# Kernel optimization log

Hardware: AMD Instinct MI355X
Metric: run time of the kernel (lower is better)

Reference implementation:

```python
import jax, jax.numpy as jnp
import numpy as np

LAGRANGE_ORDER = 5  # fixed, as in the torch module


def _lagrange_weights(alpha):
    """Vectorised Lagrange weights of length L+1. alpha: [B,N] -> [B,N,L+1]."""
    L = LAGRANGE_ORDER
    j = jnp.arange(L + 1, dtype=alpha.dtype)
    u = alpha[..., None] - j                          # [B,N,L+1]
    denom = j[:, None] - j[None, :]                   # [L+1,L+1]
    mask = ~jnp.eye(L + 1, dtype=bool)
    num = jnp.where(mask, u[..., None, :], jnp.ones_like(u)[..., None, :])
    den = jnp.where(mask, denom, jnp.ones_like(denom))
    return (num / den).prod(axis=-1)                  # [B,N,L+1]


def setup_inputs() -> dict:
    key = jax.random.key(0)
    k1, k2, k3 = jax.random.split(key, 3)
    B, N = 16, 16384
    # fractional period in samples, in [40, 100) -> max floor(f0)=99, K=99+5+3=107<=108
    f0 = 40.0 + 60.0 * jax.random.uniform(k1, (B, N), dtype=jnp.float32)
    x = jax.random.normal(k2, (B, N), dtype=jnp.float32)
    l_b = jax.random.uniform(k3, (B, N, 2), dtype=jnp.float32)  # (g, p) in [0,1]
    return {"f0": f0, "x": x, "l_b": l_b, "K": 108}


def reference(f0, x, l_b, K):
    B, N = x.shape
    L = LAGRANGE_ORDER
    # design_loop: (g, p) -> loop taps [b0, a1]; gain capped <1 for stability
    g = 0.99 * l_b[..., 0]
    p = l_b[..., 1]
    b0 = g * (1.0 - p)                                # [B,N]
    a1 = g * p
    # tune_f0: subtract low-frequency phase delay of (b0 + a1 z^-1)
    f0c = f0 - a1 / (b0 + a1 + 1e-7)
    # Lagrange centre & weights
    z = jnp.floor(f0c).astype(jnp.int32)
    z_center = z - L // 2                             # [B,N]
    alpha = f0c - z_center.astype(f0.dtype)
    w = _lagrange_weights(alpha)                      # [B,N,L+1]
    # compute_resonator_matrix: loop filter convolved with fractional delay -> block [B,N,L+2]
    block = (b0[..., None] * jnp.pad(w, ((0, 0), (0, 0), (0, 1)))
             + a1[..., None] * jnp.pad(w, ((0, 0), (0, 0), (1, 0))))
    # scatter (-block) into A; LPC lag k+1 lives in column k
    cols = z_center[..., None] - 1 + jnp.arange(L + 2)  # [B,N,L+2]
    cols = jnp.clip(cols, 0, K - 1)
    A = jnp.zeros((B, N, K), x.dtype).at[
        jnp.arange(B)[:, None, None], jnp.arange(N)[None, :, None], cols
    ].add(-block)
    # sample_wise_lpc: y[n] = x[n] - sum_k A[n,k] * y[n-1-k], zero init state
    def step(buf, inp):
        a_n, x_n = inp                                 # [B,K], [B]
        y_n = x_n - jnp.sum(a_n * buf, axis=-1)
        buf = jnp.concatenate([y_n[:, None], buf[:, :-1]], axis=1)
        return buf, y_n
    buf0 = jnp.zeros((B, K), x.dtype)
    _, ys = jax.lax.scan(step, buf0, (A.transpose(1, 0, 2), x.T))  # ys: [N,B]
    return ys.T
```

## Files before the change

kernel.cpp:

```cpp
#include <hip/hip_runtime.h>
#include <math.h>


#define B_    16
#define N_    16384
#define S_    16
#define NSEG  1024
#define NITER 28
#define RUNS  104
#define CHUNK 37
#define RSTR  108

#define CW_FLOATS (B_ * N_ * 8)
#define TG_FLOATS (B_ * S_ * RUNS * RUNS)
#define ST_FLOATS (B_ * S_ * RUNS)

__device__ __forceinline__ void diffks_coeffs(float f0v, float lbg, float lbp,
                                              int n, float4& lo, float4& hi) {
  float g  = 0.99f * lbg;
  float p  = lbp;
  float b0 = g * (1.0f - p);
  float a1 = g * p;
  float f0c = f0v - a1 / (b0 + a1 + 1e-7f);
  int   zc  = (int)floorf(f0c) - 2;
  float alpha = f0c - (float)zc;
  float u0 = alpha;
  float u1 = alpha - 1.0f;
  float u2 = alpha - 2.0f;
  float u3 = alpha - 3.0f;
  float u4 = alpha - 4.0f;
  float u5 = alpha - 5.0f;
  float w0 = u1 * u2 * u3 * u4 * u5 * (-1.0f / 120.0f);
  float w1 = u0 * u2 * u3 * u4 * u5 * ( 1.0f /  24.0f);
  float w2 = u0 * u1 * u3 * u4 * u5 * (-1.0f /  12.0f);
  float w3 = u0 * u1 * u2 * u4 * u5 * ( 1.0f /  12.0f);
  float w4 = u0 * u1 * u2 * u3 * u5 * (-1.0f /  24.0f);
  float w5 = u0 * u1 * u2 * u3 * u4 * ( 1.0f / 120.0f);
  lo.x = b0 * w0;
  lo.y = fmaf(b0, w1, a1 * w0);
  lo.z = fmaf(b0, w2, a1 * w1);
  lo.w = fmaf(b0, w3, a1 * w2);
  hi.x = fmaf(b0, w4, a1 * w3);
  hi.y = fmaf(b0, w5, a1 * w4);
  hi.z = a1 * w5;
  hi.w = __int_as_float((n - 6 - zc) & 255);
}

__global__ __launch_bounds__(832) void diffks_phase1(
    const float* __restrict__ f0, const float* __restrict__ lb,
    const float* __restrict__ x, float* __restrict__ Tg) {
  const int bs = blockIdx.x;
  const int b  = bs >> 4, s = bs & 15;
  const int n0 = s << 10;
  const int tid = threadIdx.x;

  __shared__ __align__(16) float hist[256 * RSTR];
  __shared__ float4 stA[NSEG], stB[NSEG];
  __shared__ float  stX[NSEG];

  for (int i = tid; i < 256 * RSTR; i += 832) hist[i] = 0.0f;
  for (int i = tid; i < NSEG; i += 832) {
    const int n = n0 + i;
    const size_t gi = (size_t)b * N_ + n;
    float4 lo, hi;
    diffks_coeffs(f0[gi], lb[2 * gi], lb[2 * gi + 1], n, lo, hi);
    stA[i] = lo; stB[i] = hi; stX[i] = x[gi];
  }
  __syncthreads();
  if (tid < 103) hist[(103 - tid) * RSTR + tid] = 1.0f;
  __syncthreads();

  const int w  = tid >> 6;
  const int ln = tid & 63;
  const int l  = ln & 31;
  const int h  = ln >> 5;
  const int c0 = 8 * w + 4 * h;
  const bool px = (w == 12) && (h == 1);

  for (int t = 0; t < 32; ++t) {
    const int p = 32 * t + l;
    const float4 lo = stA[p];
    const float4 hi = stB[p];
    const int base1 = (__float_as_int(hi.w) + 104) & 255;
    float4 acc;
    acc.x = 0.0f; acc.y = 0.0f; acc.z = 0.0f;
    acc.w = px ? stX[p] : 0.0f;
    const float c[7] = {hi.z, hi.y, hi.x, lo.w, lo.z, lo.y, lo.x};
#pragma unroll
    for (int m = 0; m < 7; ++m) {
      const int row = (base1 + m) & 255;
      const float4 v = *(const float4*)&hist[row * RSTR + c0];
      acc.x = fmaf(c[m], v.x, acc.x);
      acc.y = fmaf(c[m], v.y, acc.y);
      acc.z = fmaf(c[m], v.z, acc.z);
      acc.w = fmaf(c[m], v.w, acc.w);
    }
    *(float4*)&hist[((p + 104) & 255) * RSTR + c0] = acc;
    __builtin_amdgcn_wave_barrier();
    asm volatile("" ::: "memory");
  }
  __syncthreads();

  float* __restrict__ T = Tg + (size_t)bs * RUNS * RUNS;
  for (int idx = tid; idx < RUNS * RUNS; idx += 832) {
    const int r = idx / RUNS;
    const int j = idx - r * RUNS;
    T[idx] = (j < 103) ? hist[((103 - j) & 255) * RSTR + r] : 0.0f;
  }
}

__global__ __launch_bounds__(832) void diffks_phase2(
    const float* __restrict__ Tg, float* __restrict__ states) {
  const int b   = blockIdx.x;
  const int tid = threadIdx.x;
  const int j   = tid % RUNS;
  const int q   = tid / RUNS;
  const int r0  = 13 * q;
  __shared__ float cur[RUNS];
  __shared__ float part[8][105];
  if (tid < 103) cur[tid] = 0.0f;
  if (tid == 103) cur[103] = 1.0f;
  __syncthreads();

  const float* __restrict__ Tb = Tg + (size_t)b * S_ * RUNS * RUNS;
  float tv[13];
#pragma unroll
  for (int k = 0; k < 13; ++k)
    tv[k] = Tb[(size_t)(r0 + k) * RUNS + j];

  for (int s = 0; s < S_; ++s) {
    if (q == 0) states[((size_t)b * S_ + s) * RUNS + j] = cur[j];
    float acc = 0.0f;
#pragma unroll
    for (int k = 0; k < 13; ++k) acc = fmaf(tv[k], cur[r0 + k], acc);
    if (s + 1 < S_) {
      const float* __restrict__ Tn = Tb + (size_t)(s + 1) * RUNS * RUNS;
#pragma unroll
      for (int k = 0; k < 13; ++k)
        tv[k] = Tn[(size_t)(r0 + k) * RUNS + j];
    }
    part[q][j] = acc;
    __syncthreads();
    if (q == 0) {
      float v = 0.0f;
#pragma unroll
      for (int qq = 0; qq < 8; ++qq) v += part[qq][j];
      cur[j] = (j < 103) ? v : 1.0f;
    }
    __syncthreads();
  }
}

__global__ __launch_bounds__(256) void diffks_phase3(
    const float* __restrict__ f0, const float* __restrict__ lb,
    const float* __restrict__ x, const float* __restrict__ states,
    float* __restrict__ y) {
  const int bs = blockIdx.x;
  const int b  = bs >> 4, s = bs & 15;
  const int n0 = s << 10;
  const int tid = threadIdx.x;

  __shared__ __align__(16) float ring[512];
  __shared__ float4 sC[2 * NSEG];
  __shared__ float  sX[NSEG];
  __shared__ float  sY[NSEG];

  for (int i = tid; i < 512; i += 256) ring[i] = 0.0f;
  for (int i = tid; i < NSEG; i += 256) {
    const int n = n0 + i;
    const size_t gi = (size_t)b * N_ + n;
    float4 lo, hi;
    diffks_coeffs(f0[gi], lb[2 * gi], lb[2 * gi + 1], n, lo, hi);
    sC[2 * i] = lo; sC[2 * i + 1] = hi; sX[i] = x[gi];
  }
  __syncthreads();
  const float* __restrict__ st = states + (size_t)bs * RUNS;
  for (int k = tid; k < 103; k += 256) {
    const float v = st[k];
    ring[255 - k] = v;
    ring[511 - k] = v;
  }
  __syncthreads();

  if (tid < 64) {
    const int lane = tid;
    const bool act = (lane < CHUNK);
    for (int t = 0; t < NITER; ++t) {
      const int p = t * CHUNK + lane;
      if (act && p < NSEG) {
        const float4 lo = sC[2 * p];
        const float4 hi = sC[2 * p + 1];
        const float  xv = sX[p];
        const int base = __float_as_int(hi.w);
        const float r0 = ring[base + 0];
        const float r1 = ring[base + 1];
        const float r2 = ring[base + 2];
        const float r3 = ring[base + 3];
        const float r4 = ring[base + 4];
        const float r5 = ring[base + 5];
        const float r6 = ring[base + 6];
        const float s0 = fmaf(lo.x, r6, xv);
        const float s1 = fmaf(lo.y, r5, lo.z * r4);
        const float s2 = fmaf(lo.w, r3, hi.x * r2);
        const float s3 = fmaf(hi.y, r1, hi.z * r0);
        const float yv = (s0 + s1) + (s2 + s3);
        const int wsl = p & 255;
        ring[wsl]       = yv;
        ring[wsl + 256] = yv;
        sY[p] = yv;
      }
      __builtin_amdgcn_wave_barrier();
      asm volatile("" ::: "memory");
    }
  }
  __syncthreads();

  float4* __restrict__ yb = (float4*)(y + (size_t)b * N_ + n0);
  yb[tid] = ((const float4*)sY)[tid];
}

__global__ __launch_bounds__(256) void diffks_coeff_fb(
    const float* __restrict__ f0, const float* __restrict__ lb,
    float* __restrict__ cw, int total, int Nmask) {
  int idx = blockIdx.x * blockDim.x + threadIdx.x;
  if (idx >= total) return;
  float4 lo, hi;
  diffks_coeffs(f0[idx], lb[2 * idx], lb[2 * idx + 1], idx & Nmask, lo, hi);
  float4* out4 = (float4*)cw;
  out4[2 * idx]     = lo;
  out4[2 * idx + 1] = hi;
}

__global__ __launch_bounds__(64) void diffks_scan_fb(
    const float* __restrict__ x, const float* __restrict__ cw,
    float* __restrict__ y, int N) {
  const int b    = blockIdx.x;
  const int lane = threadIdx.x;
  __shared__ float ring[512];
#pragma unroll
  for (int i = 0; i < 8; ++i) ring[lane + 64 * i] = 0.0f;
  __builtin_amdgcn_wave_barrier();
  asm volatile("" ::: "memory");
  const float4* __restrict__ c4 = (const float4*)(cw + (size_t)b * N * 8);
  const float*  __restrict__ xb = x + (size_t)b * N;
  float*        __restrict__ yb = y + (size_t)b * N;
  const bool act = (lane < CHUNK);
  const int nIter = (N + CHUNK - 1) / CHUNK;
  for (int t = 0; t < nIter; ++t) {
    const int n = t * CHUNK + lane;
    if (act && n < N) {
      const float4 lo = c4[2 * n];
      const float4 hi = c4[2 * n + 1];
      const float  xv = xb[n];
      const int base = __float_as_int(hi.w);
      const float r0 = ring[base + 0];
      const float r1 = ring[base + 1];
      const float r2 = ring[base + 2];
      const float r3 = ring[base + 3];
      const float r4 = ring[base + 4];
      const float r5 = ring[base + 5];
      const float r6 = ring[base + 6];
      const float s0 = fmaf(lo.x, r6, xv);
      const float s1 = fmaf(lo.y, r5, lo.z * r4);
      const float s2 = fmaf(lo.w, r3, hi.x * r2);
      const float s3 = fmaf(hi.y, r1, hi.z * r0);
      const float yv = (s0 + s1) + (s2 + s3);
      ring[n & 255]         = yv;
      ring[(n & 255) + 256] = yv;
      yb[n] = yv;
    }
    __builtin_amdgcn_wave_barrier();
    asm volatile("" ::: "memory");
  }
}

extern "C" void kernel_launch(void* const* d_in, const int* in_sizes, int n_in,
                              void* d_out, int out_size, void* d_ws, size_t ws_size,
                              hipStream_t stream) {
  const float* f0 = (const float*)d_in[0];
  const float* x  = (const float*)d_in[1];
  const float* lb = (const float*)d_in[2];
  float* out = (float*)d_out;

  const int total = in_sizes[0];
  const size_t need = (size_t)(TG_FLOATS + ST_FLOATS) * 4;

  if (total == B_ * N_ && ws_size >= need) {
    float* Tg = (float*)d_ws;
    float* st = Tg + TG_FLOATS;
    diffks_phase1<<<B_ * S_, 832, 0, stream>>>(f0, lb, x, Tg);
    diffks_phase2<<<B_, 832, 0, stream>>>(Tg, st);
    diffks_phase3<<<B_ * S_, 256, 0, stream>>>(f0, lb, x, st, out);
  } else {
    const int N = total / B_;
    float* cw = (float*)d_ws;
    diffks_coeff_fb<<<(total + 255) / 256, 256, 0, stream>>>(f0, lb, cw, total, N - 1);
    diffks_scan_fb<<<B_, 64, 0, stream>>>(x, cw, out, N);
  }
}
```

Baseline: 111.2 us.

## Compute coefficients inline with register prefetch; shrink hist zeroing; double-buffer phase2 loads

Phase1 no longer precomputes per-sample coefficients into shared staging arrays. Each lane prefetches the next sample's f0, loop params and x into registers and computes the Lagrange/loop coefficients inside the serial recurrence loop. This removes the shared staging arrays and a pass over shared memory, at the cost of extra ALU work on the sequential critical path. The hist zeroing is vectorised to float4 stores, and phase2 now prefetches two segments ahead using two register buffers to hide global load latency.

```diff
diff --git a/kernel.cpp b/kernel.cpp
--- a/kernel.cpp
+++ b/kernel.cpp
@@ -11,7 +11,6 @@
 #define CHUNK 37
 #define RSTR  108
 
-#define CW_FLOATS (B_ * N_ * 8)
 #define TG_FLOATS (B_ * S_ * RUNS * RUNS)
 #define ST_FLOATS (B_ * S_ * RUNS)
 
@@ -55,17 +54,9 @@
   const int tid = threadIdx.x;
 
   __shared__ __align__(16) float hist[256 * RSTR];
-  __shared__ float4 stA[NSEG], stB[NSEG];
-  __shared__ float  stX[NSEG];
-
-  for (int i = tid; i < 256 * RSTR; i += 832) hist[i] = 0.0f;
-  for (int i = tid; i < NSEG; i += 832) {
-    const int n = n0 + i;
-    const size_t gi = (size_t)b * N_ + n;
-    float4 lo, hi;
-    diffks_coeffs(f0[gi], lb[2 * gi], lb[2 * gi + 1], n, lo, hi);
-    stA[i] = lo; stB[i] = hi; stX[i] = x[gi];
-  }
+
+  for (int i = tid; i < 64 * RSTR; i += 832)
+    ((float4*)hist)[i] = float4{0.0f, 0.0f, 0.0f, 0.0f};
   __syncthreads();
   if (tid < 103) hist[(103 - tid) * RSTR + tid] = 1.0f;
   __syncthreads();
@@ -77,14 +68,31 @@
   const int c0 = 8 * w + 4 * h;
   const bool px = (w == 12) && (h == 1);
 
+  const size_t gb = (size_t)b * N_ + n0;
+  const float*  __restrict__ f0b = f0 + gb;
+  const float2* __restrict__ lbb = (const float2*)(lb + 2 * gb);
+  const float*  __restrict__ xb  = x + gb;
+
+  float  nf0 = f0b[l];
+  float2 nlb = lbb[l];
+  float  nx  = xb[l];
+
   for (int t = 0; t < 32; ++t) {
     const int p = 32 * t + l;
-    const float4 lo = stA[p];
-    const float4 hi = stB[p];
+    const float  cf0 = nf0;
+    const float2 clb = nlb;
+    const float  cx  = nx;
+    if (t < 31) {
+      nf0 = f0b[p + 32];
+      nlb = lbb[p + 32];
+      nx  = xb[p + 32];
+    }
+    float4 lo, hi;
+    diffks_coeffs(cf0, clb.x, clb.y, p, lo, hi);
     const int base1 = (__float_as_int(hi.w) + 104) & 255;
     float4 acc;
     acc.x = 0.0f; acc.y = 0.0f; acc.z = 0.0f;
-    acc.w = px ? stX[p] : 0.0f;
+    acc.w = px ? cx : 0.0f;
     const float c[7] = {hi.z, hi.y, hi.x, lo.w, lo.z, lo.y, lo.x};
 #pragma unroll
     for (int m = 0; m < 7; ++m) {
@@ -123,18 +131,22 @@
   __syncthreads();
 
   const float* __restrict__ Tb = Tg + (size_t)b * S_ * RUNS * RUNS;
-  float tv[13];
-#pragma unroll
-  for (int k = 0; k < 13; ++k)
-    tv[k] = Tb[(size_t)(r0 + k) * RUNS + j];
-
+  float tvA[13], tvB[13];
+#pragma unroll
+  for (int k = 0; k < 13; ++k) {
+    tvA[k] = Tb[(size_t)(r0 + k) * RUNS + j];
+    tvB[k] = Tb[(size_t)RUNS * RUNS + (size_t)(r0 + k) * RUNS + j];
+  }
+
+#pragma unroll
   for (int s = 0; s < S_; ++s) {
+    float* tv = (s & 1) ? tvB : tvA;
     if (q == 0) states[((size_t)b * S_ + s) * RUNS + j] = cur[j];
     float acc = 0.0f;
 #pragma unroll
     for (int k = 0; k < 13; ++k) acc = fmaf(tv[k], cur[r0 + k], acc);
-    if (s + 1 < S_) {
-      const float* __restrict__ Tn = Tb + (size_t)(s + 1) * RUNS * RUNS;
+    if (s + 2 < S_) {
+      const float* __restrict__ Tn = Tb + (size_t)(s + 2) * RUNS * RUNS;
 #pragma unroll
       for (int k = 0; k < 13; ++k)
         tv[k] = Tn[(size_t)(r0 + k) * RUNS + j];
```

Result: no change. 112.5 us (+1.2%).
